# Performance work log

Hardware: AMD Instinct MI355X
Metric: run time of the kernel (lower is better)

The kernel has to match this reference:

```python
import jax, jax.numpy as jnp
import numpy as np

MAX_POS = 1024  # config.max_position_embeddings
NUM_HEADS = 16
HEAD_DIM = 64


def setup_inputs() -> dict:
    key = jax.random.key(0)
    ks = jax.random.split(key, 4)
    B, S, H = 4, 1024, 1024
    return {
        "hidden_states": jax.random.normal(ks[0], (B, S, H), dtype=jnp.float32),
        "qkv_w": jax.random.normal(ks[1], (3 * H, H), dtype=jnp.float32) * 0.02,
        "qkv_b": jax.random.normal(ks[2], (3 * H,), dtype=jnp.float32) * 0.02,
        "dist_emb": jax.random.normal(ks[3], (2 * MAX_POS - 1, HEAD_DIM), dtype=jnp.float32) * 0.02,
        "ext_mask": jnp.zeros((B, 1, 1, S), dtype=jnp.float32),
    }


def reference(hidden_states, qkv_w, qkv_b, dist_emb, ext_mask):
    B, S, H = hidden_states.shape
    h, d = NUM_HEADS, HEAD_DIM
    # fused QKV projection (q|k|v concatenated on output dim)
    qkv = jnp.einsum('bsi,oi->bso', hidden_states, qkv_w) + qkv_b
    q, k, v = jnp.split(qkv, 3, axis=-1)
    to_heads = lambda x: x.reshape(B, S, h, d).transpose(0, 2, 1, 3)  # [B,h,S,d]
    q, k, v = to_heads(q), to_heads(k), to_heads(v)
    # raw attention scores [B,h,S,S]
    scores = jnp.einsum('bhld,bhrd->bhlr', q, k)
    # relative_key_query positional bias
    pos = jnp.arange(S)
    distance = pos[:, None] - pos[None, :]          # [S,S]
    pe = dist_emb[distance + MAX_POS - 1]           # [S,S,d]
    scores = scores + jnp.einsum('bhld,lrd->bhlr', q, pe) \
                    + jnp.einsum('bhrd,lrd->bhlr', k, pe)
    scores = scores / jnp.sqrt(jnp.asarray(d, scores.dtype))
    scores = scores + ext_mask
    probs = jax.nn.softmax(scores, axis=-1)
    ctx = jnp.einsum('bhlr,bhrd->bhld', probs, v)   # [B,h,S,d]
    return ctx.transpose(0, 2, 1, 3).reshape(B, S, h * d)
```

## Files before the change

kernel.cpp:

```cpp
#include <hip/hip_runtime.h>

#define SEQ 1024
#define NH  16

typedef __attribute__((ext_vector_type(8))) short short8;
typedef __attribute__((ext_vector_type(4))) float floatx4;
typedef __attribute__((ext_vector_type(4))) unsigned short ushortx4;

#define GLDS16(gp, lp) __builtin_amdgcn_global_load_lds( \
    (const __attribute__((address_space(1))) void*)(gp), \
    (__attribute__((address_space(3))) void*)(lp), 16, 0, 0)

__device__ __forceinline__ unsigned short f2b(float f) {
    union { float f; unsigned u; } v; v.f = f;
    unsigned r = (v.u + 0x7fffu + ((v.u >> 16) & 1u)) >> 16;
    return (unsigned short)r;
}
__device__ __forceinline__ float b2f(unsigned short h) {
    union { unsigned u; float f; } v; v.u = ((unsigned)h) << 16;
    return v.f;
}

#define TADDR(base, row, ch) ((base) + ((row) << 6) + ((((ch) ^ ((row) & 7))) << 3))

__global__ void cast_kernel(const float* __restrict__ hs, const float* __restrict__ W,
                            const float* __restrict__ E,
                            unsigned short* __restrict__ hsb,
                            unsigned short* __restrict__ Wb,
                            unsigned short* __restrict__ Eb)
{
    const int QH = 1048576, QW = 786432, QE = 32752;
    const int NT = QH + QW + QE;
    for (int q = blockIdx.x * 256 + threadIdx.x; q < NT; q += gridDim.x * 256) {
        const float* src; unsigned short* dst; int off;
        if (q < QH)           { src = hs; dst = hsb; off = q; }
        else if (q < QH + QW) { src = W;  dst = Wb;  off = q - QH; }
        else                  { src = E;  dst = Eb;  off = q - QH - QW; }
        const float4 v = *(const float4*)(src + (size_t)off * 4);
        ushortx4 o; o[0] = f2b(v.x); o[1] = f2b(v.y); o[2] = f2b(v.z); o[3] = f2b(v.w);
        *(ushortx4*)(dst + (size_t)off * 4) = o;
    }
}

__global__ __launch_bounds__(256, 3) void qkv_gemm(
    const unsigned short* __restrict__ Ab, const unsigned short* __restrict__ Bb,
    const float* __restrict__ bias,
    unsigned short* __restrict__ Qb, unsigned short* __restrict__ Kb,
    unsigned short* __restrict__ Vt)
{
    __shared__ unsigned short sm[16384];
    const int t = threadIdx.x, w = t >> 6;
    const int ln = t & 15, g = (t >> 4) & 3;
    const int wm = w >> 1, wn = w & 1;
    const int bid = blockIdx.x + blockIdx.y * 24;
    const int swzid = (bid & 7) * 96 + (bid >> 3);
    const int m0 = (swzid / 24) << 7, o0 = (swzid % 24) << 7;

    floatx4 acc[4][4];
#pragma unroll
    for (int i = 0; i < 4; ++i)
#pragma unroll
        for (int j = 0; j < 4; ++j) acc[i][j] = (floatx4){0.f, 0.f, 0.f, 0.f};

    auto stage = [&](int kb, int buf) {
        const int base = buf << 14;
#pragma unroll
        for (int p = 0; p < 2; ++p) {
            const int idx = (p << 8) + t;
            const int row = idx >> 2;
            const int c = (idx & 3) ^ ((row ^ (row >> 2)) & 3);
            GLDS16(Ab + (size_t)(m0 + row) * 1024 + kb + (c << 3),
                   (char*)sm + base + (p << 12) + (w << 10));
            GLDS16(Bb + (size_t)(o0 + row) * 1024 + kb + (c << 3),
                   (char*)sm + base + 8192 + (p << 12) + (w << 10));
        }
    };

    stage(0, 0);
    __syncthreads();
    int buf = 0;
    for (int kb = 0; kb < 1024; kb += 32) {
        if (kb + 32 < 1024) stage(kb + 32, buf ^ 1);
        const int be = buf << 13;
        short8 af[4], bf_[4];
#pragma unroll
        for (int i = 0; i < 4; ++i) {
            const int r = (wm << 6) + (i << 4) + ln;
            af[i] = *(const short8*)&sm[be + (r << 5) + ((g ^ ((r ^ (r >> 2)) & 3)) << 3)];
        }
#pragma unroll
        for (int j = 0; j < 4; ++j) {
            const int r = (wn << 6) + (j << 4) + ln;
            bf_[j] = *(const short8*)&sm[be + 4096 + (r << 5) + ((g ^ ((r ^ (r >> 2)) & 3)) << 3)];
        }
#pragma unroll
        for (int i = 0; i < 4; ++i)
#pragma unroll
            for (int j = 0; j < 4; ++j)
                acc[i][j] = __builtin_amdgcn_mfma_f32_16x16x32_bf16(af[i], bf_[j], acc[i][j], 0, 0, 0);
        __syncthreads();
        buf ^= 1;
    }

    const int which = o0 >> 10;
    float bj[4];
#pragma unroll
    for (int j = 0; j < 4; ++j) bj[j] = bias[o0 + (wn << 6) + (j << 4) + ln];

    if (which == 2) {
#pragma unroll
        for (int i = 0; i < 4; ++i) {
            const int m = m0 + (wm << 6) + (i << 4) + (g << 2);
            const int b = m >> 10, s = m & 1023;
#pragma unroll
            for (int j = 0; j < 4; ++j) {
                const int o = o0 + (wn << 6) + (j << 4) + ln;
                const int d = o & 63, hh = (o >> 6) & 15;
                ushortx4 pk;
#pragma unroll
                for (int q = 0; q < 4; ++q) pk[q] = f2b(acc[i][j][q] + bj[j]);
                *(ushortx4*)(Vt + (((size_t)((b << 4) + hh)) << 16) + (d << 10) + s) = pk;
            }
        }
    } else {
        unsigned short* dst = which ? Kb : Qb;
        const float sc = which ? 1.0f : 0.125f;
#pragma unroll
        for (int i = 0; i < 4; ++i)
#pragma unroll
            for (int q = 0; q < 4; ++q) {
                const int m = m0 + (wm << 6) + (i << 4) + (g << 2) + q;
                const int b = m >> 10, s = m & 1023;
#pragma unroll
                for (int j = 0; j < 4; ++j) {
                    const int o = o0 + (wn << 6) + (j << 4) + ln;
                    const int d = o & 63, hh = (o >> 6) & 15;
                    dst[(((size_t)((b << 4) + hh)) << 16) + (s << 6) + d] =
                        f2b((acc[i][j][q] + bj[j]) * sc);
                }
            }
    }
}

__global__ __launch_bounds__(256, 3) void attn_mfma(
    const unsigned short* __restrict__ Qb, const unsigned short* __restrict__ Kb,
    const unsigned short* __restrict__ Vt, const unsigned short* __restrict__ Eb,
    const float* __restrict__ mask, float* __restrict__ outp)
{
    __shared__ __align__(16) unsigned short sm[25600];
    const int t = threadIdx.x, w = t >> 6;
    const int wu = __builtin_amdgcn_readfirstlane(w);
    const int ln = t & 15, g = (t >> 4) & 3;
    const int bid = blockIdx.x;
    const int swz = ((bid & 7) << 7) | (bid >> 3);
    const int bh = swz >> 4;
    const int l0 = (swz & 15) << 6;
    const int b = bh >> 4, h = bh & 15;
    const size_t hb = (size_t)bh << 16;
    const int x0 = (w << 4) + (g << 2);

    const int qr = (w << 4) + ln;
    const short8 qa0 = *(const short8*)(Qb + hb + ((size_t)(l0 + qr) << 6) + (g << 3));
    const short8 qa1 = *(const short8*)(Qb + hb + ((size_t)(l0 + qr) << 6) + 32 + (g << 3));

    floatx4 O[4];
    float mr[4], lr[4];
#pragma unroll
    for (int dt = 0; dt < 4; ++dt) O[dt] = (floatx4){0.f, 0.f, 0.f, 0.f};
#pragma unroll
    for (int q = 0; q < 4; ++q) { mr[q] = -1e30f; lr[q] = 0.f; }

    for (int r0 = 0; r0 < SEQ; r0 += 64) {
        float mk4[4];
#pragma unroll
        for (int j = 0; j < 4; ++j) mk4[j] = mask[(b << 10) + r0 + (j << 4) + ln];

        __syncthreads();
#pragma unroll
        for (int p = 0; p < 2; ++p) {
            const int idx = (p << 8) + t;
            const int row = idx >> 3;
            const int c = (idx & 7) ^ (row & 7);
            GLDS16(Kb + hb + ((size_t)(r0 + row) << 6) + (c << 3),
                   (char*)sm + (p << 12) + (w << 10));
        }
        const int j0 = l0 - r0 + 960;
#pragma unroll
        for (int p = 0; p < 4; ++p) {
            const int idx = (p << 8) + t;
            const int row = idx >> 3;
            const int c = (idx & 7) ^ (row & 7);
            GLDS16(Eb + ((size_t)(j0 + row) << 6) + (c << 3),
                   (char*)sm + 8192 + (p << 12) + (w << 10));
        }
        __syncthreads();
        short8 kf[4][2];
#pragma unroll
        for (int j = 0; j < 4; ++j) {
            const int kr = (j << 4) + ln;
            kf[j][0] = *(const short8*)&sm[TADDR(0, kr, g)];
            kf[j][1] = *(const short8*)&sm[TADDR(0, kr, 4 + g)];
        }
        const int wr = (w << 4) + ln;
        const short8 ka0 = *(const short8*)&sm[TADDR(0, wr, g)];
        const short8 ka1 = *(const short8*)&sm[TADDR(0, wr, 4 + g)];

        __builtin_amdgcn_s_setprio(1);
        floatx4 S[4];
#pragma unroll
        for (int j = 0; j < 4; ++j) {
            floatx4 z = (floatx4){0.f, 0.f, 0.f, 0.f};
            z = __builtin_amdgcn_mfma_f32_16x16x32_bf16(qa0, kf[j][0], z, 0, 0, 0);
            S[j] = __builtin_amdgcn_mfma_f32_16x16x32_bf16(qa1, kf[j][1], z, 0, 0, 0);
        }
#pragma unroll
        for (int dt = 0; dt < 8; ++dt) {
            const bool doU = (dt >= wu) && (dt <= wu + 4);
            const bool doW = (dt >= 3 - wu) && (dt <= 7 - wu);
            if (!doU && !doW) continue;
            const int er = (dt << 4) + ln;
            const short8 e0 = *(const short8*)&sm[TADDR(4096, er, g)];
            const short8 e1 = *(const short8*)&sm[TADDR(4096, er, 4 + g)];
            if (doU) {
                floatx4 z = (floatx4){0.f, 0.f, 0.f, 0.f};
                z = __builtin_amdgcn_mfma_f32_16x16x32_bf16(qa0, e0, z, 0, 0, 0);
                const floatx4 U = __builtin_amdgcn_mfma_f32_16x16x32_bf16(qa1, e1, z, 0, 0, 0);
                int a = 12288 + (x0 - (dt << 4) - ln + 79) * 72 + x0;
#pragma unroll
                for (int q = 0; q < 4; ++q) { sm[a] = f2b(U[q]); a += 73; }
            }
            if (doW) {
                floatx4 z2 = (floatx4){0.f, 0.f, 0.f, 0.f};
                z2 = __builtin_amdgcn_mfma_f32_16x16x32_bf16(ka0, e0, z2, 0, 0, 0);
                const floatx4 Wv = __builtin_amdgcn_mfma_f32_16x16x32_bf16(ka1, e1, z2, 0, 0, 0);
                int a = 19200 + x0 * 101 + (dt << 4) + ln - 47;
#pragma unroll
                for (int q = 0; q < 4; ++q) { sm[a] = f2b(Wv[q] * 0.125f); a += 101; }
            }
        }
        __builtin_amdgcn_s_setprio(0);
        __syncthreads();
#pragma unroll
        for (int p = 0; p < 2; ++p) {
            const int idx = (p << 8) + t;
            const int row = idx >> 3;
            const int c = (idx & 7) ^ (row & 7);
            GLDS16(Vt + hb + ((size_t)row << 10) + r0 + (c << 3),
                   (char*)sm + 8192 + (p << 12) + (w << 10));
        }
        float Pw[4][4];
#pragma unroll
        for (int j = 0; j < 4; ++j) {
            const int rr = (j << 4) + ln;
            const ushortx4 u4 = *(const ushortx4*)&sm[12288 + (rr + 16) * 72 + x0];
            const ushortx4 w4 = *(const ushortx4*)&sm[19200 + rr * 100 + 16 + x0];
#pragma unroll
            for (int q = 0; q < 4; ++q)
                S[j][q] += b2f(u4[q]) + b2f(w4[q]) + mk4[j];
        }
#pragma unroll
        for (int q = 0; q < 4; ++q) {
            float tm = fmaxf(fmaxf(S[0][q], S[1][q]), fmaxf(S[2][q], S[3][q]));
            tm = fmaxf(tm, __shfl_xor(tm, 1));
            tm = fmaxf(tm, __shfl_xor(tm, 2));
            tm = fmaxf(tm, __shfl_xor(tm, 4));
            tm = fmaxf(tm, __shfl_xor(tm, 8));
            const float mnew = fmaxf(mr[q], tm);
            const float al = __expf(mr[q] - mnew);
            float sum = 0.f;
#pragma unroll
            for (int j = 0; j < 4; ++j) {
                const float p = __expf(S[j][q] - mnew);
                Pw[j][q] = p; sum += p;
            }
            sum += __shfl_xor(sum, 1);
            sum += __shfl_xor(sum, 2);
            sum += __shfl_xor(sum, 4);
            sum += __shfl_xor(sum, 8);
            lr[q] = lr[q] * al + sum;
            mr[q] = mnew;
#pragma unroll
            for (int dt = 0; dt < 4; ++dt) O[dt][q] *= al;
        }
#pragma unroll
        for (int j = 0; j < 4; ++j) {
            const int rr = (j << 4) + ln;
#pragma unroll
            for (int q = 0; q < 4; ++q) {
                const int l = x0 + q;
                sm[8192 + (l << 6) + ((((rr >> 3) ^ (l & 7)) << 3)) + (rr & 7)] = f2b(Pw[j][q]);
            }
        }
        __syncthreads();
        const int pr = (w << 4) + ln;
        const short8 pa0 = *(const short8*)&sm[TADDR(8192, pr, g)];
        const short8 pa1 = *(const short8*)&sm[TADDR(8192, pr, 4 + g)];
        __builtin_amdgcn_s_setprio(1);
#pragma unroll
        for (int dt = 0; dt < 4; ++dt) {
            const int vr = (dt << 4) + ln;
            const short8 v0 = *(const short8*)&sm[TADDR(4096, vr, g)];
            const short8 v1 = *(const short8*)&sm[TADDR(4096, vr, 4 + g)];
            O[dt] = __builtin_amdgcn_mfma_f32_16x16x32_bf16(pa0, v0, O[dt], 0, 0, 0);
            O[dt] = __builtin_amdgcn_mfma_f32_16x16x32_bf16(pa1, v1, O[dt], 0, 0, 0);
        }
        __builtin_amdgcn_s_setprio(0);
    }
#pragma unroll
    for (int dt = 0; dt < 4; ++dt)
#pragma unroll
        for (int q = 0; q < 4; ++q) {
            const int l = x0 + q;
            outp[((size_t)b << 20) + ((size_t)(l0 + l) << 10) + (h << 6) + (dt << 4) + ln]
                = O[dt][q] / lr[q];
        }
}

extern "C" void kernel_launch(void* const* d_in, const int* in_sizes, int n_in,
                              void* d_out, int out_size, void* d_ws, size_t ws_size,
                              hipStream_t stream)
{
    const float* hs   = (const float*)d_in[0];
    const float* qkvw = (const float*)d_in[1];
    const float* qkvb = (const float*)d_in[2];
    const float* demb = (const float*)d_in[3];
    const float* mask = (const float*)d_in[4];
    float* out = (float*)d_out;

    char* ws = (char*)d_ws;
    unsigned short* hsb = (unsigned short*)(ws);
    unsigned short* Wb  = (unsigned short*)(ws + 8388608);
    unsigned short* Eb  = (unsigned short*)(ws + 14680064);
    unsigned short* Qb  = (unsigned short*)(ws + 14942208);
    unsigned short* Kb  = (unsigned short*)(ws + 23330816);
    unsigned short* Vt  = (unsigned short*)(ws + 31719424);

    cast_kernel<<<2048, 256, 0, stream>>>(hs, qkvw, demb, hsb, Wb, Eb);
    qkv_gemm<<<dim3(24, 32), 256, 0, stream>>>(hsb, Wb, qkvb, Qb, Kb, Vt);
    attn_mfma<<<1024, 256, 0, stream>>>(Qb, Kb, Vt, Eb, mask, out);
}
```

Before: 234.5 us.

## Stage QKV GEMM epilogue through LDS for coalesced 16-byte stores; drop setprio

After: 229.8 us. 1.02x faster.

```diff
diff --git a/kernel.cpp b/kernel.cpp
--- a/kernel.cpp
+++ b/kernel.cpp
@@ -106,21 +106,32 @@
     float bj[4];
 #pragma unroll
     for (int j = 0; j < 4; ++j) bj[j] = bias[o0 + (wn << 6) + (j << 4) + ln];
+    const int b0 = m0 >> 10;
 
     if (which == 2) {
 #pragma unroll
-        for (int i = 0; i < 4; ++i) {
-            const int m = m0 + (wm << 6) + (i << 4) + (g << 2);
-            const int b = m >> 10, s = m & 1023;
+        for (int i = 0; i < 4; ++i)
 #pragma unroll
             for (int j = 0; j < 4; ++j) {
-                const int o = o0 + (wn << 6) + (j << 4) + ln;
-                const int d = o & 63, hh = (o >> 6) & 15;
-                ushortx4 pk;
-#pragma unroll
-                for (int q = 0; q < 4; ++q) pk[q] = f2b(acc[i][j][q] + bj[j]);
-                *(ushortx4*)(Vt + (((size_t)((b << 4) + hh)) << 16) + (d << 10) + s) = pk;
-            }
+                const int oi = (wn << 6) + (j << 4) + ln;
+                const int sb = oi & 15;
+#pragma unroll
+                for (int q = 0; q < 4; ++q) {
+                    const int mi = (wm << 6) + (i << 4) + (g << 2) + q;
+                    sm[(oi << 7) + ((((mi >> 3) ^ sb)) << 3) + (mi & 7)] =
+                        f2b(acc[i][j][q] + bj[j]);
+                }
+            }
+        __syncthreads();
+#pragma unroll
+        for (int it = 0; it < 8; ++it) {
+            const int c = (it << 8) + t;
+            const int oi = c >> 4, mi0 = (c & 15) << 3;
+            const short8 v = *(const short8*)&sm[(oi << 7) + ((((mi0 >> 3) ^ (oi & 15))) << 3)];
+            const int hh = ((o0 >> 6) + (oi >> 6)) & 15;
+            const int d = oi & 63;
+            const int s0 = (m0 & 1023) + mi0;
+            *(short8*)(Vt + (((size_t)((b0 << 4) + hh)) << 16) + (d << 10) + s0) = v;
         }
     } else {
         unsigned short* dst = which ? Kb : Qb;
@@ -128,17 +139,25 @@
 #pragma unroll
         for (int i = 0; i < 4; ++i)
 #pragma unroll
-            for (int q = 0; q < 4; ++q) {
-                const int m = m0 + (wm << 6) + (i << 4) + (g << 2) + q;
-                const int b = m >> 10, s = m & 1023;
-#pragma unroll
-                for (int j = 0; j < 4; ++j) {
-                    const int o = o0 + (wn << 6) + (j << 4) + ln;
-                    const int d = o & 63, hh = (o >> 6) & 15;
-                    dst[(((size_t)((b << 4) + hh)) << 16) + (s << 6) + d] =
-                        f2b((acc[i][j][q] + bj[j]) * sc);
+            for (int j = 0; j < 4; ++j) {
+                const int oi = (wn << 6) + (j << 4) + ln;
+#pragma unroll
+                for (int q = 0; q < 4; ++q) {
+                    const int mi = (wm << 6) + (i << 4) + (g << 2) + q;
+                    sm[(mi << 7) + oi] = f2b((acc[i][j][q] + bj[j]) * sc);
                 }
             }
+        __syncthreads();
+#pragma unroll
+        for (int it = 0; it < 8; ++it) {
+            const int c = (it << 8) + t;
+            const int mi = c >> 4, oi0 = (c & 15) << 3;
+            const short8 v = *(const short8*)&sm[(mi << 7) + oi0];
+            const int s = (m0 & 1023) + mi;
+            const int hh = ((o0 >> 6) + (oi0 >> 6)) & 15;
+            const int d0 = oi0 & 63;
+            *(short8*)(dst + (((size_t)((b0 << 4) + hh)) << 16) + (s << 6) + d0) = v;
+        }
     }
 }
 
@@ -171,10 +190,6 @@
     for (int q = 0; q < 4; ++q) { mr[q] = -1e30f; lr[q] = 0.f; }
 
     for (int r0 = 0; r0 < SEQ; r0 += 64) {
-        float mk4[4];
-#pragma unroll
-        for (int j = 0; j < 4; ++j) mk4[j] = mask[(b << 10) + r0 + (j << 4) + ln];
-
         __syncthreads();
 #pragma unroll
         for (int p = 0; p < 2; ++p) {
@@ -205,7 +220,6 @@
         const short8 ka0 = *(const short8*)&sm[TADDR(0, wr, g)];
         const short8 ka1 = *(const short8*)&sm[TADDR(0, wr, 4 + g)];
 
-        __builtin_amdgcn_s_setprio(1);
         floatx4 S[4];
 #pragma unroll
         for (int j = 0; j < 4; ++j) {
@@ -238,7 +252,6 @@
                 for (int q = 0; q < 4; ++q) { sm[a] = f2b(Wv[q] * 0.125f); a += 101; }
             }
         }
-        __builtin_amdgcn_s_setprio(0);
         __syncthreads();
 #pragma unroll
         for (int p = 0; p < 2; ++p) {
@@ -252,11 +265,12 @@
 #pragma unroll
         for (int j = 0; j < 4; ++j) {
             const int rr = (j << 4) + ln;
+            const float mk = mask[(b << 10) + r0 + rr];
             const ushortx4 u4 = *(const ushortx4*)&sm[12288 + (rr + 16) * 72 + x0];
             const ushortx4 w4 = *(const ushortx4*)&sm[19200 + rr * 100 + 16 + x0];
 #pragma unroll
             for (int q = 0; q < 4; ++q)
-                S[j][q] += b2f(u4[q]) + b2f(w4[q]) + mk4[j];
+                S[j][q] += b2f(u4[q]) + b2f(w4[q]) + mk;
         }
 #pragma unroll
         for (int q = 0; q < 4; ++q) {
@@ -295,7 +309,6 @@
         const int pr = (w << 4) + ln;
         const short8 pa0 = *(const short8*)&sm[TADDR(8192, pr, g)];
         const short8 pa1 = *(const short8*)&sm[TADDR(8192, pr, 4 + g)];
-        __builtin_amdgcn_s_setprio(1);
 #pragma unroll
         for (int dt = 0; dt < 4; ++dt) {
             const int vr = (dt << 4) + ln;
@@ -304,7 +317,6 @@
             O[dt] = __builtin_amdgcn_mfma_f32_16x16x32_bf16(pa0, v0, O[dt], 0, 0, 0);
             O[dt] = __builtin_amdgcn_mfma_f32_16x16x32_bf16(pa1, v1, O[dt], 0, 0, 0);
         }
-        __builtin_amdgcn_s_setprio(0);
     }
 #pragma unroll
     for (int dt = 0; dt < 4; ++dt)
```
